# Optimization experiments

Measured on AMD Instinct MI355X. Metric: run time of the kernel, lower is better.

The kernel has to match this reference:

```python
import jax, jax.numpy as jnp
import numpy as np

DIM = 384
HEADS = 6
EPS = 1e-5
SCALE = DIM ** -0.5  # note: original uses full dim, not head_dim


def _dwconv_bn(x, w, stride, g, b, m, v):
    # x: [B, C, H, W], w: [C, 1, 3, 3] depthwise
    y = jax.lax.conv_general_dilated(
        x, w, window_strides=(stride, stride), padding=((1, 1), (1, 1)),
        dimension_numbers=('NCHW', 'OIHW', 'NCHW'), feature_group_count=DIM)
    # BatchNorm2d inference form
    inv = jax.lax.rsqrt(v + EPS)
    y = (y - m[None, :, None, None]) * (inv * g)[None, :, None, None] + b[None, :, None, None]
    # b c h w -> b (h w) c
    B, C, H, W = y.shape
    return y.reshape(B, C, H * W).transpose(0, 2, 1)


def setup_inputs() -> dict:
    key = jax.random.key(0)
    ks = jax.random.split(key, 24)
    d = {}
    d['x'] = jax.random.normal(ks[0], (8, 3136, DIM), jnp.float32)
    d['h'] = 56
    d['w'] = 56
    i = 1
    for nm in ('q', 'k', 'v'):
        d[f'conv_{nm}'] = jax.random.normal(ks[i], (DIM, 1, 3, 3), jnp.float32) * 0.1; i += 1
        d[f'bn{nm}_s'] = jnp.ones((DIM,), jnp.float32)
        d[f'bn{nm}_b'] = jnp.zeros((DIM,), jnp.float32)
        d[f'bn{nm}_m'] = jax.random.normal(ks[i], (DIM,), jnp.float32) * 0.1; i += 1
        d[f'bn{nm}_v'] = jax.random.uniform(ks[i], (DIM,), jnp.float32) + 0.5; i += 1
    s = DIM ** -0.5
    d['wq'] = jax.random.normal(ks[i], (DIM, DIM), jnp.float32) * s; i += 1
    d['wk'] = jax.random.normal(ks[i], (DIM, DIM), jnp.float32) * s; i += 1
    d['wv'] = jax.random.normal(ks[i], (DIM, DIM), jnp.float32) * s; i += 1
    d['w_last'] = jax.random.normal(ks[i], (DIM, DIM), jnp.float32) * s; i += 1
    d['b_last'] = jnp.zeros((DIM,), jnp.float32)
    return d


def reference(x, h, w, conv_q, bnq_s, bnq_b, bnq_m, bnq_v,
              conv_k, bnk_s, bnk_b, bnk_m, bnk_v,
              conv_v, bnv_s, bnv_b, bnv_m, bnv_v,
              wq, wk, wv, w_last, b_last):
    B, T, C = x.shape
    xim = x.transpose(0, 2, 1).reshape(B, C, h, w)  # b (h w) c -> b c h w
    q = _dwconv_bn(xim, conv_q, 1, bnq_s, bnq_b, bnq_m, bnq_v)  # [B, h*w, C]
    k = _dwconv_bn(xim, conv_k, 2, bnk_s, bnk_b, bnk_m, bnk_v)  # [B, hw/4, C]
    v = _dwconv_bn(xim, conv_v, 2, bnv_s, bnv_b, bnv_m, bnv_v)
    # linear projections (torch Linear: y = x @ W.T), split heads
    def heads(t, W):
        y = jnp.einsum('btc,oc->bto', t, W)
        Bt, Tt, _ = y.shape
        return y.reshape(Bt, Tt, HEADS, C // HEADS).transpose(0, 2, 1, 3)
    qh, kh, vh = heads(q, wq), heads(k, wk), heads(v, wv)
    attn = jax.nn.softmax(jnp.einsum('bhld,bhtd->bhlt', qh, kh) * SCALE, axis=-1)
    o = jnp.einsum('bhlt,bhtd->bhld', attn, vh)  # [B, H, L, d]
    o = o.transpose(0, 2, 1, 3).reshape(B, T, C)
    return jnp.einsum('btc,oc->bto', o, w_last) + b_last
```

## Files before the change

kernel.cpp:

```cpp
#include <hip/hip_runtime.h>
#include <hip/hip_bf16.h>

typedef __bf16 bf16;
typedef __attribute__((ext_vector_type(8))) __bf16 bf16x8;
typedef __attribute__((ext_vector_type(4))) __bf16 bf16x4;
typedef __attribute__((ext_vector_type(2))) __bf16 bf16x2;
typedef __attribute__((ext_vector_type(4))) float floatx4;
typedef __attribute__((ext_vector_type(16))) float floatx16;
typedef unsigned int u32;

#define MFMA16(a, b, c) __builtin_amdgcn_mfma_f32_16x16x32_bf16((a), (b), (c), 0, 0, 0)
#define MFMA32(a, b, c) __builtin_amdgcn_mfma_f32_32x32x16_bf16((a), (b), (c), 0, 0, 0)

#define DIM 384
#define T1 3136
#define T2 784
#define T2P 832
#define B_ 8
#define EPSV 1e-5f

__device__ __forceinline__ void gload_lds16(const bf16* g, bf16* l) {
  __builtin_amdgcn_global_load_lds(
      (const __attribute__((address_space(1))) void*)g,
      (__attribute__((address_space(3))) void*)l, 16, 0, 0);
}

__device__ __forceinline__ u32 pk2(float a, float b) {
  bf16x2 t = (bf16x2){(bf16)a, (bf16)b};
  return *reinterpret_cast<u32*>(&t);
}

__global__ void conv_fused_kernel(const float* __restrict__ x,
    const float* __restrict__ wqc, const float* __restrict__ gq, const float* __restrict__ bq,
    const float* __restrict__ mq, const float* __restrict__ vq,
    const float* __restrict__ wkc, const float* __restrict__ gk, const float* __restrict__ bk,
    const float* __restrict__ mk, const float* __restrict__ vk,
    const float* __restrict__ wvc, const float* __restrict__ gv, const float* __restrict__ bv,
    const float* __restrict__ mv, const float* __restrict__ vvv,
    bf16* __restrict__ qout, bf16* __restrict__ kout, bf16* __restrict__ vout,
    const float* __restrict__ w0, const float* __restrict__ w1,
    const float* __restrict__ w2, const float* __restrict__ w3,
    bf16* __restrict__ d0, bf16* __restrict__ d1,
    bf16* __restrict__ d2, bf16* __restrict__ d3) {
  int blk = blockIdx.x;
  int c = threadIdx.x;
  int gid = blk * DIM + c;
  if (gid < 147456) {
    d0[gid] = (bf16)w0[gid]; d1[gid] = (bf16)w1[gid];
    d2[gid] = (bf16)w2[gid]; d3[gid] = (bf16)w3[gid];
  }
  int xg = blk % 14;
  int y = (blk / 14) % 56;
  int b = blk / (14 * 56);
  int x0 = xg * 4;
  const float* xb = x + (size_t)b * T1 * DIM;
  float in[3][6];
#pragma unroll
  for (int r = 0; r < 3; ++r) {
    int yy = y + r - 1;
#pragma unroll
    for (int cc = 0; cc < 6; ++cc) {
      int xc = x0 + cc - 1;
      in[r][cc] = (yy >= 0 && yy < 56 && xc >= 0 && xc < 56)
                      ? xb[(yy * 56 + xc) * DIM + c] : 0.f;
    }
  }
  {
    float wr[9];
#pragma unroll
    for (int i = 0; i < 9; ++i) wr[i] = wqc[c * 9 + i];
    float a = rsqrtf(vq[c] + EPSV) * gq[c];
    float bia = bq[c] - mq[c] * a;
#pragma unroll
    for (int p = 0; p < 4; ++p) {
      float s = 0.f;
#pragma unroll
      for (int r = 0; r < 3; ++r)
#pragma unroll
        for (int dx = 0; dx < 3; ++dx) s += in[r][p + dx] * wr[r * 3 + dx];
      qout[((size_t)b * T1 + y * 56 + x0 + p) * DIM + c] = (bf16)(s * a + bia);
    }
  }
  if ((y & 1) == 0) {
    int y2 = y >> 1;
    float wk9[9], wv9[9];
#pragma unroll
    for (int i = 0; i < 9; ++i) { wk9[i] = wkc[c * 9 + i]; wv9[i] = wvc[c * 9 + i]; }
    float ak = rsqrtf(vk[c] + EPSV) * gk[c];
    float av = rsqrtf(vvv[c] + EPSV) * gv[c];
    float bik = bk[c] - mk[c] * ak;
    float biv = bv[c] - mv[c] * av;
#pragma unroll
    for (int p2 = 0; p2 < 2; ++p2) {
      float sk = 0.f, sv = 0.f;
#pragma unroll
      for (int r = 0; r < 3; ++r)
#pragma unroll
        for (int dx = 0; dx < 3; ++dx) {
          float xv = in[r][2 * p2 + dx];
          sk += xv * wk9[r * 3 + dx];
          sv += xv * wv9[r * 3 + dx];
        }
      size_t o = ((size_t)b * T2 + y2 * 28 + (x0 >> 1) + p2) * DIM + c;
      kout[o] = (bf16)(sk * ak + bik);
      vout[o] = (bf16)(sv * av + biv);
    }
  }
}

#define BK 32
#define BUFSZ (128 * BK)
__device__ __forceinline__
void gemm_body(const bf16* A, const bf16* Bw, void* out, const float* bias,
               int mode, float scale, int m0, int n0, bf16* Al, bf16* Bl) {
  int tid = threadIdx.x;
  int w = tid >> 6, lane = tid & 63;
  int wm = w >> 1, wn = w & 1;
  int l16 = lane & 15, quad = lane >> 4;
  floatx4 acc[4][4];
#pragma unroll
  for (int i = 0; i < 4; ++i)
#pragma unroll
    for (int j = 0; j < 4; ++j) acc[i][j] = (floatx4){0.f, 0.f, 0.f, 0.f};

  int srow = w * 32 + (lane >> 2);
  int scol = (lane & 3) * 8;
  const bf16* ag0 = &A[(size_t)(m0 + srow) * DIM + scol];
  const bf16* ag1 = ag0 + (size_t)16 * DIM;
  const bf16* bg0 = &Bw[(size_t)(n0 + srow) * DIM + scol];
  const bf16* bg1 = bg0 + (size_t)16 * DIM;
  int lofs0 = (w * 32) * BK;
  int lofs1 = (w * 32 + 16) * BK;

  gload_lds16(ag0, Al + lofs0);
  gload_lds16(ag1, Al + lofs1);
  gload_lds16(bg0, Bl + lofs0);
  gload_lds16(bg1, Bl + lofs1);

  const int NS = DIM / BK;
#pragma unroll
  for (int s = 0; s < NS; ++s) {
    const int cb = s & 1;
    if (s + 1 < NS) {
      const int k = (s + 1) * BK;
      bf16* an = Al + (cb ^ 1) * BUFSZ;
      bf16* bn = Bl + (cb ^ 1) * BUFSZ;
      gload_lds16(ag0 + k, an + lofs0);
      gload_lds16(ag1 + k, an + lofs1);
      gload_lds16(bg0 + k, bn + lofs0);
      gload_lds16(bg1 + k, bn + lofs1);
      asm volatile("s_waitcnt vmcnt(4)" ::: "memory");
    } else {
      asm volatile("s_waitcnt vmcnt(0)" ::: "memory");
    }
    __builtin_amdgcn_s_barrier();
    const bf16* Ac = Al + cb * BUFSZ;
    const bf16* Bc = Bl + cb * BUFSZ;
    bf16x8 af[4], bfr[4];
#pragma unroll
    for (int i = 0; i < 4; ++i) {
      af[i]  = *(const bf16x8*)&Ac[(wm * 64 + i * 16 + l16) * BK + quad * 8];
      bfr[i] = *(const bf16x8*)&Bc[(wn * 64 + i * 16 + l16) * BK + quad * 8];
    }
#pragma unroll
    for (int i = 0; i < 4; ++i)
#pragma unroll
      for (int j = 0; j < 4; ++j)
        acc[i][j] = MFMA16(af[i], bfr[j], acc[i][j]);
    asm volatile("s_waitcnt lgkmcnt(0)" ::: "memory");
    __builtin_amdgcn_s_barrier();
  }
#pragma unroll
  for (int i = 0; i < 4; ++i) {
#pragma unroll
    for (int j = 0; j < 4; ++j) {
#pragma unroll
      for (int rr = 0; rr < 4; ++rr) {
        int row = m0 + wm * 64 + i * 16 + quad * 4 + rr;
        int col = n0 + wn * 64 + j * 16 + l16;
        float v = acc[i][j][rr];
        if (mode == 3) {
          ((float*)out)[(size_t)row * DIM + col] = v + bias[col];
        } else if (mode == 2) {
          int b = row / T2;
          int t = row - b * T2;
          ((bf16*)out)[((size_t)b * DIM + col) * T2P + t] = (bf16)v;
        } else {
          ((bf16*)out)[(size_t)row * DIM + col] = (bf16)(v * scale);
        }
      }
    }
  }
}

__global__ __launch_bounds__(256)
void qkv_gemm_kernel(const bf16* q_act, const bf16* k_act, const bf16* v_act,
                     const bf16* wqb, const bf16* wkb, const bf16* wvb,
                     bf16* Qp, bf16* Kp, bf16* Vtp, float qscale) {
  __shared__ bf16 Al[2 * BUFSZ];
  __shared__ bf16 Bl[2 * BUFSZ];
  int bx = blockIdx.x;
  int xp = bx & 7, j = bx >> 3;
  int t = (j / 3) * 24 + xp * 3 + (j % 3);
  if (t >= 882) return;
  const bf16 *A, *Bw; void* out; int mode, ti; float scale;
  if (t < 588)      { A = q_act; Bw = wqb; out = Qp;  mode = 1; scale = qscale; ti = t; }
  else if (t < 735) { A = k_act; Bw = wkb; out = Kp;  mode = 0; scale = 1.f; ti = t - 588; }
  else              { A = v_act; Bw = wvb; out = Vtp; mode = 2; scale = 1.f; ti = t - 735; }
  gemm_body(A, Bw, out, nullptr, mode, scale, (ti / 3) * 128, (ti % 3) * 128, Al, Bl);
}

__global__ __launch_bounds__(256)
void last_gemm_kernel(const bf16* A, const bf16* Bw, float* out, const float* bias) {
  __shared__ bf16 Al[2 * BUFSZ];
  __shared__ bf16 Bl[2 * BUFSZ];
  int bx = blockIdx.x;
  int xp = bx & 7, j = bx >> 3;
  int t = (j / 3) * 24 + xp * 3 + (j % 3);
  if (t >= 588) return;
  gemm_body(A, Bw, out, bias, 3, 1.f, (t / 3) * 128, (t % 3) * 128, Al, Bl);
}

__global__ __launch_bounds__(256, 4)
void attn_kernel(const bf16* __restrict__ Qp, const bf16* __restrict__ Kp,
                 const bf16* __restrict__ Vt, bf16* __restrict__ Ob) {
  __shared__ bf16 Kl[64 * 64];
  __shared__ bf16 Vl[64 * 64];
  int bx = blockIdx.x;
  int xcd = bx & 7, j = bx >> 3;
  int g = xcd + 8 * (j / 25);
  int qblk = j % 25;
  int h = g % 6;
  int b = g / 6;
  int tid = threadIdx.x, w = tid >> 6, lane = tid & 63;
  int l32 = lane & 31, hi = lane >> 5;
  int q0w = qblk * 128 + w * 32;

  bf16x8 qf[4];
  {
    int qi = q0w + l32;
    qi = qi < T1 ? qi : T1 - 1;
    const bf16* qp = &Qp[((size_t)b * T1 + qi) * DIM + h * 64];
#pragma unroll
    for (int kk = 0; kk < 4; ++kk) qf[kk] = *(const bf16x8*)&qp[kk * 16 + hi * 8];
  }
  floatx16 oacc[2];
  oacc[0] = (floatx16)0.f;
  oacc[1] = (floatx16)0.f;
  float lsum = 0.f;

  int rsub = lane >> 3;
  int chnk = (lane & 7) ^ rsub;
  const bf16* kg0 = &Kp[((size_t)b * T2 + w * 16 + rsub) * DIM + h * 64 + chnk * 8];
  const bf16* kg1 = kg0 + (size_t)8 * DIM;
  const bf16* vg0 = &Vt[((size_t)b * DIM + h * 64 + w * 16 + rsub) * T2P + chnk * 8];
  const bf16* vg1 = vg0 + (size_t)8 * T2P;
  bf16* kl0 = &Kl[(w * 16) * 64];
  bf16* kl1 = &Kl[(w * 16 + 8) * 64];
  bf16* vl0 = &Vl[(w * 16) * 64];
  bf16* vl1 = &Vl[(w * 16 + 8) * 64];

  int key = lane & 7;

  for (int it = 0; it < 12; ++it) {
    __syncthreads();
    gload_lds16(kg0, kl0);
    gload_lds16(kg1, kl1);
    gload_lds16(vg0, vl0);
    gload_lds16(vg1, vl1);
    __syncthreads();
#pragma unroll
    for (int tt = 0; tt < 2; ++tt) {
      floatx16 s = (floatx16)0.f;
#pragma unroll
      for (int kk = 0; kk < 4; ++kk) {
        bf16x8 kf = *(const bf16x8*)&Kl[(tt * 32 + l32) * 64 + ((kk * 2 + hi) ^ key) * 8];
        s = MFMA32(kf, qf[kk], s);
      }
      float e[16];
#pragma unroll
      for (int r = 0; r < 16; ++r) {
        e[r] = __builtin_amdgcn_exp2f(s[r]);
        lsum += e[r];
      }
#pragma unroll
      for (int kkl = 0; kkl < 2; ++kkl) {
        int r0 = kkl * 8;
        u32 pA = pk2(e[r0 + 0], e[r0 + 1]);
        u32 pB = pk2(e[r0 + 2], e[r0 + 3]);
        u32 pC = pk2(e[r0 + 4], e[r0 + 5]);
        u32 pD = pk2(e[r0 + 6], e[r0 + 7]);
        u32 sA = __shfl_xor(pA, 32);
        u32 sB = __shfl_xor(pB, 32);
        u32 sC = __shfl_xor(pC, 32);
        u32 sD = __shfl_xor(pD, 32);
        union { u32 u[4]; bf16x8 v; } pf;
        pf.u[0] = hi ? sC : pA;
        pf.u[1] = hi ? sD : pB;
        pf.u[2] = hi ? pC : sA;
        pf.u[3] = hi ? pD : sB;
        int kk = tt * 2 + kkl;
#pragma unroll
        for (int dt = 0; dt < 2; ++dt) {
          bf16x8 vf = *(const bf16x8*)&Vl[(dt * 32 + l32) * 64 + ((kk * 2 + hi) ^ key) * 8];
          oacc[dt] = MFMA32(vf, pf.v, oacc[dt]);
        }
      }
    }
    kg0 += (size_t)64 * DIM; kg1 += (size_t)64 * DIM;
    vg0 += 64; vg1 += 64;
  }
  {
    int tq = 768 + l32;
    tq = tq < T2 ? tq : T2 - 1;
    const bf16* kp2 = &Kp[((size_t)b * T2 + tq) * DIM + h * 64];
    floatx16 s = (floatx16)0.f;
#pragma unroll
    for (int kk = 0; kk < 4; ++kk) {
      bf16x8 kf = *(const bf16x8*)&kp2[kk * 16 + hi * 8];
      s = MFMA32(kf, qf[kk], s);
    }
    float e[8];
#pragma unroll
    for (int r = 0; r < 8; ++r) {
      e[r] = __builtin_amdgcn_exp2f(s[r]);
      lsum += e[r];
    }
    u32 pA = pk2(e[0], e[1]);
    u32 pB = pk2(e[2], e[3]);
    u32 pC = pk2(e[4], e[5]);
    u32 pD = pk2(e[6], e[7]);
    u32 sA = __shfl_xor(pA, 32);
    u32 sB = __shfl_xor(pB, 32);
    u32 sC = __shfl_xor(pC, 32);
    u32 sD = __shfl_xor(pD, 32);
    union { u32 u[4]; bf16x8 v; } pf;
    pf.u[0] = hi ? sC : pA;
    pf.u[1] = hi ? sD : pB;
    pf.u[2] = hi ? pC : sA;
    pf.u[3] = hi ? pD : sB;
#pragma unroll
    for (int dt = 0; dt < 2; ++dt) {
      const bf16* vp2 = &Vt[((size_t)b * DIM + h * 64 + dt * 32 + l32) * T2P + 768 + hi * 8];
      bf16x8 vf = *(const bf16x8*)vp2;
      oacc[dt] = MFMA32(vf, pf.v, oacc[dt]);
    }
  }
  lsum += __shfl_xor(lsum, 32);
  float inv = 1.f / lsum;
  int qg = q0w + l32;
  if (qg < T1) {
    bf16* op = &Ob[((size_t)b * T1 + qg) * DIM + h * 64];
#pragma unroll
    for (int dt = 0; dt < 2; ++dt) {
#pragma unroll
      for (int gr = 0; gr < 4; ++gr) {
        bf16x4 ov = (bf16x4){(bf16)(oacc[dt][gr * 4 + 0] * inv),
                             (bf16)(oacc[dt][gr * 4 + 1] * inv),
                             (bf16)(oacc[dt][gr * 4 + 2] * inv),
                             (bf16)(oacc[dt][gr * 4 + 3] * inv)};
        *(bf16x4*)&op[dt * 32 + gr * 8 + hi * 4] = ov;
      }
    }
  }
}

extern "C" void kernel_launch(void* const* d_in, const int* in_sizes, int n_in,
                              void* d_out, int out_size, void* d_ws, size_t ws_size,
                              hipStream_t stream) {
  (void)in_sizes; (void)n_in; (void)out_size; (void)ws_size;
  const float* x      = (const float*)d_in[0];
  const float* conv_q = (const float*)d_in[3];
  const float* bnq_s  = (const float*)d_in[4];
  const float* bnq_b  = (const float*)d_in[5];
  const float* bnq_m  = (const float*)d_in[6];
  const float* bnq_v  = (const float*)d_in[7];
  const float* conv_k = (const float*)d_in[8];
  const float* bnk_s  = (const float*)d_in[9];
  const float* bnk_b  = (const float*)d_in[10];
  const float* bnk_m  = (const float*)d_in[11];
  const float* bnk_v  = (const float*)d_in[12];
  const float* conv_v = (const float*)d_in[13];
  const float* bnv_s  = (const float*)d_in[14];
  const float* bnv_b  = (const float*)d_in[15];
  const float* bnv_m  = (const float*)d_in[16];
  const float* bnv_v  = (const float*)d_in[17];
  const float* wq     = (const float*)d_in[18];
  const float* wk     = (const float*)d_in[19];
  const float* wv     = (const float*)d_in[20];
  const float* wl     = (const float*)d_in[21];
  const float* b_last = (const float*)d_in[22];

  char* ws = (char*)d_ws;
  bf16* q_act = (bf16*)(ws + 0);
  bf16* k_act = (bf16*)(ws + 19267584);
  bf16* v_act = (bf16*)(ws + 24084480);
  bf16* Qp    = (bf16*)(ws + 28901376);
  bf16* Kp    = (bf16*)(ws + 48168960);
  bf16* Vtp   = (bf16*)(ws + 52985856);
  bf16* wqb   = (bf16*)(ws + 58097664);
  bf16* wkb   = wqb + 147456;
  bf16* wvb   = wkb + 147456;
  bf16* wlb   = wvb + 147456;

  const float QSCALE = 0.05103103630798288f * 1.4426950408889634f;

  conv_fused_kernel<<<B_ * 56 * 14, DIM, 0, stream>>>(
      x,
      conv_q, bnq_s, bnq_b, bnq_m, bnq_v,
      conv_k, bnk_s, bnk_b, bnk_m, bnk_v,
      conv_v, bnv_s, bnv_b, bnv_m, bnv_v,
      q_act, k_act, v_act,
      wq, wk, wv, wl, wqb, wkb, wvb, wlb);

  qkv_gemm_kernel<<<888, 256, 0, stream>>>(q_act, k_act, v_act, wqb, wkb, wvb,
                                           Qp, Kp, Vtp, QSCALE);

  attn_kernel<<<25 * 6 * B_, 256, 0, stream>>>(Qp, Kp, Vtp, q_act);

  last_gemm_kernel<<<600, 256, 0, stream>>>(q_act, wlb, (float*)d_out, b_last);
}
```

Measured before the change: 247.8 us.

## Enlarge projection GEMM tiles to 256x128 with 32x32 MFMA and swizzled LDS

Replaces the 128x128 tile, BK=32, 16x16x32 MFMA GEMM body with a 512-thread 256x128 tile using BK=64 and 32x32x16 MFMA instructions. LDS chunks are XOR-swizzled by row to avoid bank conflicts on fragment reads. Output stores for K and V are bounds-checked because the K/V row count no longer divides the tile height. The aim is more operand reuse per LDS load and fewer instructions, at the cost of fewer, larger blocks (about 444 and 294) and higher register and LDS pressure per block.

```diff
diff --git a/kernel.cpp b/kernel.cpp
--- a/kernel.cpp
+++ b/kernel.cpp
@@ -5,11 +5,9 @@
 typedef __attribute__((ext_vector_type(8))) __bf16 bf16x8;
 typedef __attribute__((ext_vector_type(4))) __bf16 bf16x4;
 typedef __attribute__((ext_vector_type(2))) __bf16 bf16x2;
-typedef __attribute__((ext_vector_type(4))) float floatx4;
 typedef __attribute__((ext_vector_type(16))) float floatx16;
 typedef unsigned int u32;
 
-#define MFMA16(a, b, c) __builtin_amdgcn_mfma_f32_16x16x32_bf16((a), (b), (c), 0, 0, 0)
 #define MFMA32(a, b, c) __builtin_amdgcn_mfma_f32_32x32x16_bf16((a), (b), (c), 0, 0, 0)
 
 #define DIM 384
@@ -108,83 +106,98 @@
   }
 }
 
-#define BK 32
-#define BUFSZ (128 * BK)
+#define BK64 64
+#define ABUF (256 * BK64)
+#define BBUF (128 * BK64)
 __device__ __forceinline__
-void gemm_body(const bf16* A, const bf16* Bw, void* out, const float* bias,
-               int mode, float scale, int m0, int n0, bf16* Al, bf16* Bl) {
+void gemm512_body(const bf16* A, const bf16* Bw, void* out, const float* bias,
+                  int mode, float scale, int m0, int n0, int Mrows,
+                  bf16* Al, bf16* Bl) {
   int tid = threadIdx.x;
   int w = tid >> 6, lane = tid & 63;
   int wm = w >> 1, wn = w & 1;
-  int l16 = lane & 15, quad = lane >> 4;
-  floatx4 acc[4][4];
-#pragma unroll
-  for (int i = 0; i < 4; ++i)
-#pragma unroll
-    for (int j = 0; j < 4; ++j) acc[i][j] = (floatx4){0.f, 0.f, 0.f, 0.f};
-
-  int srow = w * 32 + (lane >> 2);
-  int scol = (lane & 3) * 8;
-  const bf16* ag0 = &A[(size_t)(m0 + srow) * DIM + scol];
-  const bf16* ag1 = ag0 + (size_t)16 * DIM;
-  const bf16* bg0 = &Bw[(size_t)(n0 + srow) * DIM + scol];
-  const bf16* bg1 = bg0 + (size_t)16 * DIM;
-  int lofs0 = (w * 32) * BK;
-  int lofs1 = (w * 32 + 16) * BK;
-
-  gload_lds16(ag0, Al + lofs0);
-  gload_lds16(ag1, Al + lofs1);
-  gload_lds16(bg0, Bl + lofs0);
-  gload_lds16(bg1, Bl + lofs1);
-
-  const int NS = DIM / BK;
+  int l32 = lane & 31, hi = lane >> 5;
+
+  int arow = lane >> 3;
+  int achk = (lane & 7) ^ arow;
+  const bf16* ag0 = &A[(size_t)(m0 + w * 32 + arow) * DIM + achk * 8];
+  const bf16* bg0 = &Bw[(size_t)(n0 + w * 16 + arow) * DIM + achk * 8];
+
+  floatx16 acc[2][2];
+  acc[0][0] = (floatx16)0.f; acc[0][1] = (floatx16)0.f;
+  acc[1][0] = (floatx16)0.f; acc[1][1] = (floatx16)0.f;
+
+  auto STAGE = [&](int s) {
+    int bi = s & 1;
+    int k = s * BK64;
+    bf16* ad = Al + bi * ABUF + (w * 32) * BK64;
+    bf16* bd = Bl + bi * BBUF + (w * 16) * BK64;
+    gload_lds16(ag0 + k, ad);
+    gload_lds16(ag0 + (size_t)8 * DIM + k, ad + 8 * BK64);
+    gload_lds16(ag0 + (size_t)16 * DIM + k, ad + 16 * BK64);
+    gload_lds16(ag0 + (size_t)24 * DIM + k, ad + 24 * BK64);
+    gload_lds16(bg0 + k, bd);
+    gload_lds16(bg0 + (size_t)8 * DIM + k, bd + 8 * BK64);
+  };
+
+  STAGE(0);
+  const int NS = DIM / BK64;
 #pragma unroll
   for (int s = 0; s < NS; ++s) {
     const int cb = s & 1;
     if (s + 1 < NS) {
-      const int k = (s + 1) * BK;
-      bf16* an = Al + (cb ^ 1) * BUFSZ;
-      bf16* bn = Bl + (cb ^ 1) * BUFSZ;
-      gload_lds16(ag0 + k, an + lofs0);
-      gload_lds16(ag1 + k, an + lofs1);
-      gload_lds16(bg0 + k, bn + lofs0);
-      gload_lds16(bg1 + k, bn + lofs1);
-      asm volatile("s_waitcnt vmcnt(4)" ::: "memory");
+      STAGE(s + 1);
+      asm volatile("s_waitcnt vmcnt(6)" ::: "memory");
     } else {
       asm volatile("s_waitcnt vmcnt(0)" ::: "memory");
     }
     __builtin_amdgcn_s_barrier();
-    const bf16* Ac = Al + cb * BUFSZ;
-    const bf16* Bc = Bl + cb * BUFSZ;
-    bf16x8 af[4], bfr[4];
-#pragma unroll
-    for (int i = 0; i < 4; ++i) {
-      af[i]  = *(const bf16x8*)&Ac[(wm * 64 + i * 16 + l16) * BK + quad * 8];
-      bfr[i] = *(const bf16x8*)&Bc[(wn * 64 + i * 16 + l16) * BK + quad * 8];
-    }
-#pragma unroll
-    for (int i = 0; i < 4; ++i)
-#pragma unroll
-      for (int j = 0; j < 4; ++j)
-        acc[i][j] = MFMA16(af[i], bfr[j], acc[i][j]);
+    const bf16* Ac = Al + cb * ABUF;
+    const bf16* Bc = Bl + cb * BBUF;
+#pragma unroll
+    for (int ksp = 0; ksp < 2; ++ksp) {
+      bf16x8 af[2][2], bfr[2][2];
+#pragma unroll
+      for (int kh = 0; kh < 2; ++kh) {
+        int ks = ksp * 2 + kh;
+        int ch = ((ks * 2 + hi) ^ (l32 & 7)) * 8;
+#pragma unroll
+        for (int mt = 0; mt < 2; ++mt)
+          af[mt][kh] = *(const bf16x8*)&Ac[(wm * 64 + mt * 32 + l32) * BK64 + ch];
+#pragma unroll
+        for (int nt = 0; nt < 2; ++nt)
+          bfr[nt][kh] = *(const bf16x8*)&Bc[(wn * 64 + nt * 32 + l32) * BK64 + ch];
+      }
+#pragma unroll
+      for (int kh = 0; kh < 2; ++kh)
+#pragma unroll
+        for (int mt = 0; mt < 2; ++mt)
+#pragma unroll
+          for (int nt = 0; nt < 2; ++nt)
+            acc[mt][nt] = MFMA32(af[mt][kh], bfr[nt][kh], acc[mt][nt]);
+    }
     asm volatile("s_waitcnt lgkmcnt(0)" ::: "memory");
     __builtin_amdgcn_s_barrier();
   }
 #pragma unroll
-  for (int i = 0; i < 4; ++i) {
-#pragma unroll
-    for (int j = 0; j < 4; ++j) {
-#pragma unroll
-      for (int rr = 0; rr < 4; ++rr) {
-        int row = m0 + wm * 64 + i * 16 + quad * 4 + rr;
-        int col = n0 + wn * 64 + j * 16 + l16;
-        float v = acc[i][j][rr];
+  for (int mt = 0; mt < 2; ++mt) {
+#pragma unroll
+    for (int nt = 0; nt < 2; ++nt) {
+      int col = n0 + wn * 64 + nt * 32 + l32;
+#pragma unroll
+      for (int r = 0; r < 16; ++r) {
+        int row = m0 + wm * 64 + mt * 32 + (r & 3) + 8 * (r >> 2) + 4 * hi;
+        float v = acc[mt][nt][r];
         if (mode == 3) {
           ((float*)out)[(size_t)row * DIM + col] = v + bias[col];
         } else if (mode == 2) {
-          int b = row / T2;
-          int t = row - b * T2;
-          ((bf16*)out)[((size_t)b * DIM + col) * T2P + t] = (bf16)v;
+          if (row < Mrows) {
+            int b = row / T2;
+            int t = row - b * T2;
+            ((bf16*)out)[((size_t)b * DIM + col) * T2P + t] = (bf16)v;
+          }
+        } else if (mode == 0) {
+          if (row < Mrows) ((bf16*)out)[(size_t)row * DIM + col] = (bf16)v;
         } else {
           ((bf16*)out)[(size_t)row * DIM + col] = (bf16)(v * scale);
         }
@@ -193,32 +206,30 @@
   }
 }
 
-__global__ __launch_bounds__(256)
+__global__ __launch_bounds__(512, 2)
 void qkv_gemm_kernel(const bf16* q_act, const bf16* k_act, const bf16* v_act,
                      const bf16* wqb, const bf16* wkb, const bf16* wvb,
                      bf16* Qp, bf16* Kp, bf16* Vtp, float qscale) {
-  __shared__ bf16 Al[2 * BUFSZ];
-  __shared__ bf16 Bl[2 * BUFSZ];
+  __shared__ bf16 Al[2 * ABUF];
+  __shared__ bf16 Bl[2 * BBUF];
   int bx = blockIdx.x;
-  int xp = bx & 7, j = bx >> 3;
-  int t = (j / 3) * 24 + xp * 3 + (j % 3);
-  if (t >= 882) return;
-  const bf16 *A, *Bw; void* out; int mode, ti; float scale;
-  if (t < 588)      { A = q_act; Bw = wqb; out = Qp;  mode = 1; scale = qscale; ti = t; }
-  else if (t < 735) { A = k_act; Bw = wkb; out = Kp;  mode = 0; scale = 1.f; ti = t - 588; }
-  else              { A = v_act; Bw = wvb; out = Vtp; mode = 2; scale = 1.f; ti = t - 735; }
-  gemm_body(A, Bw, out, nullptr, mode, scale, (ti / 3) * 128, (ti % 3) * 128, Al, Bl);
-}
-
-__global__ __launch_bounds__(256)
+  int t = (bx & 7) * 56 + (bx >> 3);
+  if (t >= 444) return;
+  const bf16 *A, *Bw; void* out; int mode, ti, M; float scale = 1.f;
+  if (t < 294)      { A = q_act; Bw = wqb; out = Qp;  mode = 1; ti = t;       M = T1 * B_; scale = qscale; }
+  else if (t < 369) { A = k_act; Bw = wkb; out = Kp;  mode = 0; ti = t - 294; M = T2 * B_; }
+  else              { A = v_act; Bw = wvb; out = Vtp; mode = 2; ti = t - 369; M = T2 * B_; }
+  gemm512_body(A, Bw, out, nullptr, mode, scale, (ti / 3) * 256, (ti % 3) * 128, M, Al, Bl);
+}
+
+__global__ __launch_bounds__(512, 2)
 void last_gemm_kernel(const bf16* A, const bf16* Bw, float* out, const float* bias) {
-  __shared__ bf16 Al[2 * BUFSZ];
-  __shared__ bf16 Bl[2 * BUFSZ];
+  __shared__ bf16 Al[2 * ABUF];
+  __shared__ bf16 Bl[2 * BBUF];
   int bx = blockIdx.x;
-  int xp = bx & 7, j = bx >> 3;
-  int t = (j / 3) * 24 + xp * 3 + (j % 3);
-  if (t >= 588) return;
-  gemm_body(A, Bw, out, bias, 3, 1.f, (t / 3) * 128, (t % 3) * 128, Al, Bl);
+  int t = (bx & 7) * 37 + (bx >> 3);
+  if (t >= 294) return;
+  gemm512_body(A, Bw, out, bias, 3, 1.f, (t / 3) * 256, (t % 3) * 128, T1 * B_, Al, Bl);
 }
 
 __global__ __launch_bounds__(256, 4)
@@ -413,10 +424,10 @@
       q_act, k_act, v_act,
       wq, wk, wv, wl, wqb, wkb, wvb, wlb);
 
-  qkv_gemm_kernel<<<888, 256, 0, stream>>>(q_act, k_act, v_act, wqb, wkb, wvb,
+  qkv_gemm_kernel<<<448, 512, 0, stream>>>(q_act, k_act, v_act, wqb, wkb, wvb,
                                            Qp, Kp, Vtp, QSCALE);
 
   attn_kernel<<<25 * 6 * B_, 256, 0, stream>>>(Qp, Kp, Vtp, q_act);
 
-  last_gemm_kernel<<<600, 256, 0, stream>>>(q_act, wlb, (float*)d_out, b_last);
-}
+  last_gemm_kernel<<<296, 512, 0, stream>>>(q_act, wlb, (float*)d_out, b_last);
+}
```

Result: slower. 269.8 us (+8.9%).

## Load GEMM fragments directly from global into registers, dropping LDS staging

Applied to the files above, without the earlier changes.

The shared GEMM body no longer stages A and B tiles through LDS with global_load_lds and barriers. Each wave now loads its MFMA fragments straight from global memory into double-buffered registers, and launch bounds are raised to a minimum of two blocks per SM. This removes LDS traffic and block-level barriers. In exchange, each A and B element is reloaded by multiple waves (no reuse through shared memory), which adds global/L2 traffic, and the 16-byte row-strided loads are less coalesced.

```diff
diff --git a/kernel.cpp b/kernel.cpp
--- a/kernel.cpp
+++ b/kernel.cpp
@@ -108,11 +108,9 @@
   }
 }
 
-#define BK 32
-#define BUFSZ (128 * BK)
 __device__ __forceinline__
 void gemm_body(const bf16* A, const bf16* Bw, void* out, const float* bias,
-               int mode, float scale, int m0, int n0, bf16* Al, bf16* Bl) {
+               int mode, float scale, int m0, int n0) {
   int tid = threadIdx.x;
   int w = tid >> 6, lane = tid & 63;
   int wm = w >> 1, wn = w & 1;
@@ -123,52 +121,37 @@
 #pragma unroll
     for (int j = 0; j < 4; ++j) acc[i][j] = (floatx4){0.f, 0.f, 0.f, 0.f};
 
-  int srow = w * 32 + (lane >> 2);
-  int scol = (lane & 3) * 8;
-  const bf16* ag0 = &A[(size_t)(m0 + srow) * DIM + scol];
-  const bf16* ag1 = ag0 + (size_t)16 * DIM;
-  const bf16* bg0 = &Bw[(size_t)(n0 + srow) * DIM + scol];
-  const bf16* bg1 = bg0 + (size_t)16 * DIM;
-  int lofs0 = (w * 32) * BK;
-  int lofs1 = (w * 32 + 16) * BK;
-
-  gload_lds16(ag0, Al + lofs0);
-  gload_lds16(ag1, Al + lofs1);
-  gload_lds16(bg0, Bl + lofs0);
-  gload_lds16(bg1, Bl + lofs1);
-
-  const int NS = DIM / BK;
+  const bf16* ap[4];
+  const bf16* bp[4];
+#pragma unroll
+  for (int i = 0; i < 4; ++i) {
+    ap[i] = &A[(size_t)(m0 + wm * 64 + i * 16 + l16) * DIM + quad * 8];
+    bp[i] = &Bw[(size_t)(n0 + wn * 64 + i * 16 + l16) * DIM + quad * 8];
+  }
+
+  bf16x8 af[2][4], bfr[2][4];
+#pragma unroll
+  for (int i = 0; i < 4; ++i) {
+    af[0][i]  = *(const bf16x8*)(ap[i]);
+    bfr[0][i] = *(const bf16x8*)(bp[i]);
+  }
+  const int NS = DIM / 32;
 #pragma unroll
   for (int s = 0; s < NS; ++s) {
-    const int cb = s & 1;
+    const int cur = s & 1;
     if (s + 1 < NS) {
-      const int k = (s + 1) * BK;
-      bf16* an = Al + (cb ^ 1) * BUFSZ;
-      bf16* bn = Bl + (cb ^ 1) * BUFSZ;
-      gload_lds16(ag0 + k, an + lofs0);
-      gload_lds16(ag1 + k, an + lofs1);
-      gload_lds16(bg0 + k, bn + lofs0);
-      gload_lds16(bg1 + k, bn + lofs1);
-      asm volatile("s_waitcnt vmcnt(4)" ::: "memory");
-    } else {
-      asm volatile("s_waitcnt vmcnt(0)" ::: "memory");
-    }
-    __builtin_amdgcn_s_barrier();
-    const bf16* Ac = Al + cb * BUFSZ;
-    const bf16* Bc = Bl + cb * BUFSZ;
-    bf16x8 af[4], bfr[4];
-#pragma unroll
-    for (int i = 0; i < 4; ++i) {
-      af[i]  = *(const bf16x8*)&Ac[(wm * 64 + i * 16 + l16) * BK + quad * 8];
-      bfr[i] = *(const bf16x8*)&Bc[(wn * 64 + i * 16 + l16) * BK + quad * 8];
+      const int nk = (s + 1) * 32;
+#pragma unroll
+      for (int i = 0; i < 4; ++i) {
+        af[cur ^ 1][i]  = *(const bf16x8*)(ap[i] + nk);
+        bfr[cur ^ 1][i] = *(const bf16x8*)(bp[i] + nk);
+      }
     }
 #pragma unroll
     for (int i = 0; i < 4; ++i)
 #pragma unroll
       for (int j = 0; j < 4; ++j)
-        acc[i][j] = MFMA16(af[i], bfr[j], acc[i][j]);
-    asm volatile("s_waitcnt lgkmcnt(0)" ::: "memory");
-    __builtin_amdgcn_s_barrier();
+        acc[i][j] = MFMA16(af[cur][i], bfr[cur][j], acc[i][j]);
   }
 #pragma unroll
   for (int i = 0; i < 4; ++i) {
@@ -193,12 +176,10 @@
   }
 }
 
-__global__ __launch_bounds__(256)
+__global__ __launch_bounds__(256, 2)
 void qkv_gemm_kernel(const bf16* q_act, const bf16* k_act, const bf16* v_act,
                      const bf16* wqb, const bf16* wkb, const bf16* wvb,
                      bf16* Qp, bf16* Kp, bf16* Vtp, float qscale) {
-  __shared__ bf16 Al[2 * BUFSZ];
-  __shared__ bf16 Bl[2 * BUFSZ];
   int bx = blockIdx.x;
   int xp = bx & 7, j = bx >> 3;
   int t = (j / 3) * 24 + xp * 3 + (j % 3);
@@ -207,18 +188,16 @@
   if (t < 588)      { A = q_act; Bw = wqb; out = Qp;  mode = 1; scale = qscale; ti = t; }
   else if (t < 735) { A = k_act; Bw = wkb; out = Kp;  mode = 0; scale = 1.f; ti = t - 588; }
   else              { A = v_act; Bw = wvb; out = Vtp; mode = 2; scale = 1.f; ti = t - 735; }
-  gemm_body(A, Bw, out, nullptr, mode, scale, (ti / 3) * 128, (ti % 3) * 128, Al, Bl);
-}
-
-__global__ __launch_bounds__(256)
+  gemm_body(A, Bw, out, nullptr, mode, scale, (ti / 3) * 128, (ti % 3) * 128);
+}
+
+__global__ __launch_bounds__(256, 2)
 void last_gemm_kernel(const bf16* A, const bf16* Bw, float* out, const float* bias) {
-  __shared__ bf16 Al[2 * BUFSZ];
-  __shared__ bf16 Bl[2 * BUFSZ];
   int bx = blockIdx.x;
   int xp = bx & 7, j = bx >> 3;
   int t = (j / 3) * 24 + xp * 3 + (j % 3);
   if (t >= 588) return;
-  gemm_body(A, Bw, out, bias, 3, 1.f, (t / 3) * 128, (t % 3) * 128, Al, Bl);
+  gemm_body(A, Bw, out, bias, 3, 1.f, (t / 3) * 128, (t % 3) * 128);
 }
 
 __global__ __launch_bounds__(256, 4)
```

Result: slower. 287.3 us (+15.9%).
